# Optimization experiments

Measured on AMD Instinct MI355X. Metric: run time of the kernel, lower is better.

## Reference

```python
import jax, jax.numpy as jnp
import numpy as np

DEPTH = 6
H = 12
D = 768
FF = 4 * D
OUT_INDICES = (2, 5)
EPS = 1e-5


def layernorm(x, g, b):
    m = jnp.mean(x, axis=-1, keepdims=True)
    v = jnp.mean(jnp.square(x - m), axis=-1, keepdims=True)
    return (x - m) * jax.lax.rsqrt(v + EPS) * g + b


def setup_inputs() -> dict:
    key = jax.random.key(0)
    ks = jax.random.split(key, 8)
    B, N = 2, 1024
    s = 0.02
    inp = {
        "x": jax.random.normal(ks[0], (B, N, D), dtype=jnp.float32),
        "rel_bias": jax.random.normal(ks[1], (H, N, N), dtype=jnp.float32),
        "ln1_g": jnp.ones((DEPTH, D), jnp.float32),
        "ln1_b": jnp.zeros((DEPTH, D), jnp.float32),
        "qkv_w": jax.random.normal(ks[2], (DEPTH, D, 3 * D), dtype=jnp.float32) * s,
        "out_w": jax.random.normal(ks[3], (DEPTH, D, D), dtype=jnp.float32) * s,
        "out_b": jnp.zeros((DEPTH, D), jnp.float32),
        "ln2_g": jnp.ones((DEPTH, D), jnp.float32),
        "ln2_b": jnp.zeros((DEPTH, D), jnp.float32),
        "ff1_w": jax.random.normal(ks[4], (DEPTH, D, FF), dtype=jnp.float32) * s,
        "ff1_b": jnp.zeros((DEPTH, FF), jnp.float32),
        "ff2_w": jax.random.normal(ks[5], (DEPTH, FF, D), dtype=jnp.float32) * s,
        "ff2_b": jnp.zeros((DEPTH, D), jnp.float32),
        "lnf_g": jnp.ones((D,), jnp.float32),
        "lnf_b": jnp.zeros((D,), jnp.float32),
    }
    return inp


def reference(x, rel_bias, ln1_g, ln1_b, qkv_w, out_w, out_b, ln2_g, ln2_b,
              ff1_w, ff1_b, ff2_w, ff2_b, lnf_g, lnf_b):
    B, N, Dm = x.shape
    Dh = Dm // H
    scale = Dh ** -0.5
    kside = int(round(N ** 0.5))  # N is a perfect square (patch grid)
    feats = []
    for i in range(DEPTH):
        # --- attention block ---
        h = layernorm(x, ln1_g[i], ln1_b[i])
        qkv = h @ qkv_w[i]                                   # [B,N,3D]
        q, k, v = jnp.split(qkv, 3, axis=-1)
        q = q.reshape(B, N, H, Dh).transpose(0, 2, 1, 3)     # [B,H,N,Dh]
        k = k.reshape(B, N, H, Dh).transpose(0, 2, 1, 3)
        v = v.reshape(B, N, H, Dh).transpose(0, 2, 1, 3)
        scores = jnp.einsum('bhid,bhjd->bhij', q, k) * scale + rel_bias
        attn = jax.nn.softmax(scores, axis=-1)
        o = jnp.einsum('bhij,bhjd->bhid', attn, v)
        o = o.transpose(0, 2, 1, 3).reshape(B, N, Dm)
        x = x + (o @ out_w[i] + out_b[i])
        # --- FFN block ---
        h2 = layernorm(x, ln2_g[i], ln2_b[i])
        ff = jax.nn.gelu(h2 @ ff1_w[i] + ff1_b[i], approximate=False)
        x = x + (ff @ ff2_w[i] + ff2_b[i])
        if i in OUT_INDICES:
            feats.append(x.reshape(B, kside, kside, Dm).transpose(0, 3, 1, 2))
    xf = layernorm(x, lnf_g, lnf_b)
    return (xf, *feats)
```

## Files before the change

### kernel.cpp

```cpp
#include <hip/hip_runtime.h>
#include <hip/hip_bf16.h>

typedef unsigned short ushort_t;
typedef __attribute__((ext_vector_type(8))) __bf16 bf16x8;
typedef __attribute__((ext_vector_type(8))) unsigned short u16x8;
typedef __attribute__((ext_vector_type(4))) float f32x4;
typedef __attribute__((ext_vector_type(4))) unsigned int u32x4;

#define DEPTH 6
#define HEADS 12
#define DMODEL 768
#define FFDIM 3072
#define BATCH 2
#define SEQ 1024
#define ROWS (BATCH * SEQ)

static __device__ __forceinline__ ushort_t f2bf(float f) {
  unsigned u = __builtin_bit_cast(unsigned, f);
  u += 0x7fffu + ((u >> 16) & 1u);
  return (ushort_t)(u >> 16);
}
static __device__ __forceinline__ float bf2f(ushort_t v) {
  return __builtin_bit_cast(float, (unsigned)v << 16);
}

template <int MREP, int NREP, int EPI>
__global__ __launch_bounds__(256) void gemm_bt(
    const ushort_t* __restrict__ A, const ushort_t* __restrict__ Bt,
    int lda, int ldb, int K,
    void* __restrict__ out0, void* __restrict__ out1,
    const float* __restrict__ f0) {
  constexpr int BM = 32 * MREP;
  constexpr int BN = 32 * NREP;
  constexpr int CHA = BM / 32;
  constexpr int CHB = BN / 32;
  __shared__ ushort_t sA[2][BM * 64];
  __shared__ ushort_t sB[2][BN * 64];

  const int tid = threadIdx.x;
  const int lane = tid & 63;
  const int wid = tid >> 6;
  const int wm = wid >> 1, wn = wid & 1;

  int bx, by;
  {
    const int nb = gridDim.x * gridDim.y;
    const int bid = blockIdx.y * gridDim.x + blockIdx.x;
    const int q = nb >> 3;
    const int swz = (bid & 7) * q + (bid >> 3);
    bx = swz % gridDim.x;
    by = swz / gridDim.x;
  }

  const ushort_t* Ab = A + (long)bx * BM * lda;
  const ushort_t* Bb = Bt + (long)by * BN * ldb;

  const int srow = lane >> 3;
  const int scol = ((lane & 7) ^ srow) * 8;

  f32x4 acc[MREP][NREP];
#pragma unroll
  for (int m = 0; m < MREP; ++m)
#pragma unroll
    for (int n = 0; n < NREP; ++n) acc[m][n] = (f32x4){0.f, 0.f, 0.f, 0.f};

  const int fr = lane & 15;
  const int kq4 = lane >> 4;

  auto stage_tile = [&](int buf, int t) {
    const int k0 = t * 64;
#pragma unroll
    for (int j = 0; j < CHA; ++j) {
      const int c = wid * CHA + j;
      const ushort_t* src = Ab + (long)(c * 8 + srow) * lda + k0 + scol;
      __builtin_amdgcn_global_load_lds(
          (const __attribute__((address_space(1))) void*)src,
          (__attribute__((address_space(3))) void*)&sA[buf][c * 512], 16, 0, 0);
    }
#pragma unroll
    for (int j = 0; j < CHB; ++j) {
      const int c = wid * CHB + j;
      const ushort_t* src = Bb + (long)(c * 8 + srow) * ldb + k0 + scol;
      __builtin_amdgcn_global_load_lds(
          (const __attribute__((address_space(1))) void*)src,
          (__attribute__((address_space(3))) void*)&sB[buf][c * 512], 16, 0, 0);
    }
  };

  const int nt = K / 64;
  stage_tile(0, 0);
  for (int t = 0; t < nt; ++t) {
    const int cur = t & 1;
    asm volatile("s_waitcnt vmcnt(0)" ::: "memory");
    __builtin_amdgcn_s_barrier();
    if (t + 1 < nt) stage_tile(cur ^ 1, t + 1);
#pragma unroll
    for (int kk = 0; kk < 2; ++kk) {
      bf16x8 af[MREP], bfr[NREP];
#pragma unroll
      for (int m = 0; m < MREP; ++m) {
        const int row = wm * (MREP * 16) + m * 16 + fr;
        const int ch = (kk * 4 + kq4) ^ (row & 7);
        af[m] = *(const bf16x8*)&sA[cur][row * 64 + ch * 8];
      }
#pragma unroll
      for (int n = 0; n < NREP; ++n) {
        const int row = wn * (NREP * 16) + n * 16 + fr;
        const int ch = (kk * 4 + kq4) ^ (row & 7);
        bfr[n] = *(const bf16x8*)&sB[cur][row * 64 + ch * 8];
      }
#pragma unroll
      for (int m = 0; m < MREP; ++m)
#pragma unroll
        for (int n = 0; n < NREP; ++n)
          acc[m][n] = __builtin_amdgcn_mfma_f32_16x16x32_bf16(
              af[m], bfr[n], acc[m][n], 0, 0, 0);
    }
  }

  const long grow0 = (long)bx * BM + wm * (MREP * 16);
  const long gcol0 = (long)by * BN + wn * (NREP * 16);
  const int rr = (lane >> 4) * 4;
  const int cc = lane & 15;

#pragma unroll
  for (int m = 0; m < MREP; ++m) {
#pragma unroll
    for (int n = 0; n < NREP; ++n) {
#pragma unroll
      for (int r = 0; r < 4; ++r) {
        long row = grow0 + m * 16 + rr + r;
        long col = gcol0 + n * 16 + cc;
        float c = acc[m][n][r];
        if (EPI == 0) {
          ushort_t bv = f2bf(c);
          if (col < 1536) {
            ((ushort_t*)out0)[row * 2304 + col] = bv;
          } else {
            long h = (col - 1536) >> 6, d = (col - 1536) & 63;
            long b = row >> 10, i = row & 1023;
            ((ushort_t*)out1)[(((b * HEADS) + h) * 64 + d) * 1024 + i] = bv;
          }
        } else if (EPI == 3) {
          long idx = row * DMODEL + col;
          ((float*)out0)[idx] += c + f0[col];
        } else if (EPI == 4) {
          float t = c + f0[col];
          float g = 0.5f * t * (1.0f + erff(t * 0.70710678118f));
          ((ushort_t*)out0)[row * FFDIM + col] = f2bf(g);
        } else if (EPI == 5) {
          long idx = row * DMODEL + col;
          ((float*)out0)[idx] += c + f0[col];
        }
      }
    }
  }
}

__global__ __launch_bounds__(256) void pack_bias(const float* __restrict__ rel,
                                                 ushort_t* __restrict__ pb) {
  __shared__ ushort_t tile[1024];
  const int blk = blockIdx.x;
  const int t = blk & 15, qi = (blk >> 4) & 63, h = blk >> 10;
  const float* src = rel + ((size_t)h << 20) + (size_t)(qi * 16) * 1024 + t * 64;
  const int tid = threadIdx.x;
  const int kk = tid & 63;
#pragma unroll
  for (int it = 0; it < 4; ++it) {
    const int qr = (tid >> 6) * 4 + it;
    const float v = src[(size_t)qr * 1024 + kk];
    const int lane = (qr >> 2) * 16 + (kk & 15);
    const int idx = (kk >> 4) * 4 + (qr & 3);
    tile[lane * 16 + idx] = f2bf(v);
  }
  __syncthreads();
  ushort_t* dst = pb + (size_t)blk * 1024;
#pragma unroll
  for (int it = 0; it < 4; ++it) dst[it * 256 + tid] = tile[it * 256 + tid];
}

__global__ __launch_bounds__(128) void flash_attn(
    const ushort_t* __restrict__ qkv,
    const ushort_t* __restrict__ vt,
    const ushort_t* __restrict__ pbias,
    ushort_t* __restrict__ o) {
  __shared__ ushort_t sK[2][64 * 64];
  __shared__ ushort_t sV[2][64 * 64];
  __shared__ ushort_t sP[32 * 64];

  const int tid = threadIdx.x;
  const int lane = tid & 63;
  const int wid = tid >> 6;
  const int h = blockIdx.y, b = blockIdx.z;
  const int q0 = blockIdx.x * 32;
  const int qi = blockIdx.x * 2 + wid;

  const int fr = lane & 15;
  const int kq4 = lane >> 4;
  const int rr = kq4 * 4;
  const int cc = fr;

  const int srow = lane >> 3;
  const int scol = ((lane & 7) ^ srow) * 8;

  const ushort_t* qbase =
      qkv + (size_t)(b * 1024 + q0 + wid * 16 + fr) * 2304 + h * 64;
  bf16x8 qreg[2];
  qreg[0] = *(const bf16x8*)&qbase[kq4 * 8];
  qreg[1] = *(const bf16x8*)&qbase[32 + kq4 * 8];

  const ushort_t* Kbase = qkv + (size_t)(b * 1024) * 2304 + 768 + h * 64;
  const ushort_t* Vbase = vt + (size_t)((b * HEADS + h) * 64) * 1024;
  const ushort_t* pbb = pbias + (((size_t)h * 64 + qi) << 14) + lane * 16;

  f32x4 acc_o[4];
  float m_run[4], l_run[4];
#pragma unroll
  for (int n = 0; n < 4; ++n) acc_o[n] = (f32x4){0.f, 0.f, 0.f, 0.f};
#pragma unroll
  for (int r = 0; r < 4; ++r) { m_run[r] = -1e30f; l_run[r] = 0.f; }

  auto stage_kv = [&](int buf, int t) {
#pragma unroll
    for (int j = 0; j < 4; ++j) {
      const int c = wid * 4 + j;
      const ushort_t* src = Kbase + (size_t)(t * 64 + c * 8 + srow) * 2304 + scol;
      __builtin_amdgcn_global_load_lds(
          (const __attribute__((address_space(1))) void*)src,
          (__attribute__((address_space(3))) void*)&sK[buf][c * 512], 16, 0, 0);
    }
#pragma unroll
    for (int j = 0; j < 4; ++j) {
      const int c = wid * 4 + j;
      const ushort_t* src = Vbase + (size_t)(c * 8 + srow) * 1024 + t * 64 + scol;
      __builtin_amdgcn_global_load_lds(
          (const __attribute__((address_space(1))) void*)src,
          (__attribute__((address_space(3))) void*)&sV[buf][c * 512], 16, 0, 0);
    }
  };

  auto step = [&](int t, u16x8& bc0, u16x8& bc1, u16x8& bn0, u16x8& bn1) {
    const int cur = t & 1;
    asm volatile("s_waitcnt vmcnt(0)" ::: "memory");
    __builtin_amdgcn_s_barrier();
    if (t + 1 < 16) {
      stage_kv(cur ^ 1, t + 1);
      const ushort_t* pp = pbb + (size_t)(t + 1) * 1024;
      bn0 = *(const u16x8*)pp;
      bn1 = *(const u16x8*)(pp + 8);
    }

    f32x4 s[4];
#pragma unroll
    for (int n = 0; n < 4; ++n) s[n] = (f32x4){0.f, 0.f, 0.f, 0.f};
#pragma unroll
    for (int kk = 0; kk < 2; ++kk) {
#pragma unroll
      for (int n = 0; n < 4; ++n) {
        const int row = n * 16 + fr;
        const int ch = (kk * 4 + kq4) ^ (row & 7);
        bf16x8 kf = *(const bf16x8*)&sK[cur][row * 64 + ch * 8];
        s[n] =
            __builtin_amdgcn_mfma_f32_16x16x32_bf16(qreg[kk], kf, s[n], 0, 0, 0);
      }
    }

    float mr[4];
#pragma unroll
    for (int r = 0; r < 4; ++r) mr[r] = -1e30f;
#pragma unroll
    for (int n = 0; n < 4; ++n)
#pragma unroll
      for (int r = 0; r < 4; ++r) {
        const int idx = n * 4 + r;
        const float bv = bf2f(idx < 8 ? bc0[idx] : bc1[idx - 8]);
        float v = s[n][r] * 0.125f + bv;
        s[n][r] = v;
        mr[r] = fmaxf(mr[r], v);
      }
#pragma unroll
    for (int o_ = 1; o_ < 16; o_ <<= 1)
#pragma unroll
      for (int r = 0; r < 4; ++r) mr[r] = fmaxf(mr[r], __shfl_xor(mr[r], o_));

    float escale[4], psum[4];
#pragma unroll
    for (int r = 0; r < 4; ++r) {
      float mn = fmaxf(m_run[r], mr[r]);
      escale[r] = __expf(m_run[r] - mn);
      m_run[r] = mn;
      psum[r] = 0.f;
    }
#pragma unroll
    for (int n = 0; n < 4; ++n)
#pragma unroll
      for (int r = 0; r < 4; ++r) {
        float p = __expf(s[n][r] - m_run[r]);
        psum[r] += p;
        const int prow = wid * 16 + rr + r;
        const int pcol = n * 16 + cc;
        sP[prow * 64 + (((pcol >> 3) ^ (prow & 7)) << 3) + (pcol & 7)] = f2bf(p);
      }
#pragma unroll
    for (int o_ = 1; o_ < 16; o_ <<= 1)
#pragma unroll
      for (int r = 0; r < 4; ++r) psum[r] += __shfl_xor(psum[r], o_);
#pragma unroll
    for (int r = 0; r < 4; ++r) l_run[r] = l_run[r] * escale[r] + psum[r];

    asm volatile("s_waitcnt lgkmcnt(0)" ::: "memory");
    __builtin_amdgcn_s_barrier();

#pragma unroll
    for (int n = 0; n < 4; ++n)
#pragma unroll
      for (int r = 0; r < 4; ++r) acc_o[n][r] *= escale[r];
#pragma unroll
    for (int kk = 0; kk < 2; ++kk) {
      const int prow = wid * 16 + fr;
      const int pch = (kk * 4 + kq4) ^ (prow & 7);
      bf16x8 pf = *(const bf16x8*)&sP[prow * 64 + pch * 8];
#pragma unroll
      for (int n = 0; n < 4; ++n) {
        const int vrow = n * 16 + fr;
        const int vch = (kk * 4 + kq4) ^ (vrow & 7);
        bf16x8 vf = *(const bf16x8*)&sV[cur][vrow * 64 + vch * 8];
        acc_o[n] =
            __builtin_amdgcn_mfma_f32_16x16x32_bf16(pf, vf, acc_o[n], 0, 0, 0);
      }
    }
  };

  u16x8 bA0, bA1, bB0, bB1;
  bA0 = *(const u16x8*)pbb;
  bA1 = *(const u16x8*)(pbb + 8);
  stage_kv(0, 0);
  for (int tt = 0; tt < 16; tt += 2) {
    step(tt, bA0, bA1, bB0, bB1);
    step(tt + 1, bB0, bB1, bA0, bA1);
  }

  ushort_t* ob = o + (size_t)(b * 1024 + q0 + wid * 16) * 768 + h * 64;
#pragma unroll
  for (int r = 0; r < 4; ++r) {
    const float rinv = 1.f / l_run[r];
#pragma unroll
    for (int n = 0; n < 4; ++n)
      ob[(size_t)(rr + r) * 768 + n * 16 + cc] = f2bf(acc_o[n][r] * rinv);
  }
}

__global__ __launch_bounds__(256) void transpose_cast(
    const float* __restrict__ in, ushort_t* __restrict__ out, int R, int C) {
  __shared__ float t[32][33];
  const float* ip = in + (long)blockIdx.z * R * C;
  ushort_t* op = out + (long)blockIdx.z * R * C;
  int c0 = blockIdx.x * 32, r0 = blockIdx.y * 32;
  int tx = threadIdx.x;
  for (int i = threadIdx.y; i < 32; i += 8)
    t[i][tx] = ip[(long)(r0 + i) * C + c0 + tx];
  __syncthreads();
  for (int i = threadIdx.y; i < 32; i += 8)
    op[(long)(c0 + i) * R + r0 + tx] = f2bf(t[tx][i]);
}

__global__ __launch_bounds__(256) void ln_kernel(
    const float* __restrict__ x, const float* __restrict__ g,
    const float* __restrict__ b, void* __restrict__ out, int out_f32) {
  int row = blockIdx.x;
  int tid = threadIdx.x;
  int lane = tid & 63, wid = tid >> 6;
  const float* xr = x + (long)row * DMODEL;
  float v0 = xr[tid], v1 = xr[tid + 256], v2 = xr[tid + 512];
  float s = v0 + v1 + v2;
  __shared__ float red[8];
  for (int o = 32; o; o >>= 1) s += __shfl_xor(s, o);
  if (!lane) red[wid] = s;
  __syncthreads();
  float mean = (red[0] + red[1] + red[2] + red[3]) * (1.f / 768.f);
  float d0 = v0 - mean, d1 = v1 - mean, d2 = v2 - mean;
  float q = d0 * d0 + d1 * d1 + d2 * d2;
  for (int o = 32; o; o >>= 1) q += __shfl_xor(q, o);
  if (!lane) red[4 + wid] = q;
  __syncthreads();
  float var = (red[4] + red[5] + red[6] + red[7]) * (1.f / 768.f);
  float rs = rsqrtf(var + 1e-5f);
  float y0 = d0 * rs * g[tid] + b[tid];
  float y1 = d1 * rs * g[tid + 256] + b[tid + 256];
  float y2 = d2 * rs * g[tid + 512] + b[tid + 512];
  if (out_f32) {
    float* o_ = (float*)out + (long)row * DMODEL;
    o_[tid] = y0; o_[tid + 256] = y1; o_[tid + 512] = y2;
  } else {
    ushort_t* o_ = (ushort_t*)out + (long)row * DMODEL;
    o_[tid] = f2bf(y0); o_[tid + 256] = f2bf(y1); o_[tid + 512] = f2bf(y2);
  }
}

__global__ __launch_bounds__(256) void feat_kernel(const float* __restrict__ x,
                                                   float* __restrict__ out) {
  __shared__ float t[32][33];
  const float* xp = x + (long)blockIdx.z * SEQ * DMODEL;
  float* op = out + (long)blockIdx.z * DMODEL * SEQ;
  int n0 = blockIdx.x * 32, c0 = blockIdx.y * 32;
  int tx = threadIdx.x;
  for (int i = threadIdx.y; i < 32; i += 8)
    t[i][tx] = xp[(long)(n0 + i) * DMODEL + c0 + tx];
  __syncthreads();
  for (int i = threadIdx.y; i < 32; i += 8)
    op[(long)(c0 + i) * SEQ + n0 + tx] = t[tx][i];
}

extern "C" void kernel_launch(void* const* d_in, const int* in_sizes, int n_in,
                              void* d_out, int out_size, void* d_ws,
                              size_t ws_size, hipStream_t stream) {
  const float* x_in   = (const float*)d_in[0];
  const float* rel    = (const float*)d_in[1];
  const float* ln1_g  = (const float*)d_in[2];
  const float* ln1_b  = (const float*)d_in[3];
  const float* qkv_w  = (const float*)d_in[4];
  const float* out_w  = (const float*)d_in[5];
  const float* out_b  = (const float*)d_in[6];
  const float* ln2_g  = (const float*)d_in[7];
  const float* ln2_b  = (const float*)d_in[8];
  const float* ff1_w  = (const float*)d_in[9];
  const float* ff1_b  = (const float*)d_in[10];
  const float* ff2_w  = (const float*)d_in[11];
  const float* ff2_b  = (const float*)d_in[12];
  const float* lnf_g  = (const float*)d_in[13];
  const float* lnf_b  = (const float*)d_in[14];
  float* out = (float*)d_out;

  char* w = (char*)d_ws;
  ushort_t* wq_t = (ushort_t*)w; w += (size_t)DEPTH * 2304 * 768 * 2;
  ushort_t* wo_t = (ushort_t*)w; w += (size_t)DEPTH * 768 * 768 * 2;
  ushort_t* wf1_t = (ushort_t*)w; w += (size_t)DEPTH * 3072 * 768 * 2;
  ushort_t* wf2_t = (ushort_t*)w; w += (size_t)DEPTH * 768 * 3072 * 2;
  float* xb = (float*)w; w += (size_t)ROWS * DMODEL * 4;
  ushort_t* hb = (ushort_t*)w; w += (size_t)ROWS * DMODEL * 2;
  ushort_t* qkvb = (ushort_t*)w; w += (size_t)ROWS * 2304 * 2;
  ushort_t* vt = (ushort_t*)w; w += (size_t)BATCH * HEADS * 64 * 1024 * 2;
  ushort_t* ob = (ushort_t*)w; w += (size_t)ROWS * DMODEL * 2;
  ushort_t* ffb = (ushort_t*)w; w += (size_t)ROWS * FFDIM * 2;
  ushort_t* pbias = (ushort_t*)w; w += (size_t)HEADS * 1024 * 1024 * 2;

  dim3 tb(32, 8);
  transpose_cast<<<dim3(2304 / 32, 768 / 32, DEPTH), tb, 0, stream>>>(
      qkv_w, wq_t, 768, 2304);
  transpose_cast<<<dim3(768 / 32, 768 / 32, DEPTH), tb, 0, stream>>>(
      out_w, wo_t, 768, 768);
  transpose_cast<<<dim3(3072 / 32, 768 / 32, DEPTH), tb, 0, stream>>>(
      ff1_w, wf1_t, 768, 3072);
  transpose_cast<<<dim3(768 / 32, 3072 / 32, DEPTH), tb, 0, stream>>>(
      ff2_w, wf2_t, 3072, 768);
  pack_bias<<<HEADS * 64 * 16, 256, 0, stream>>>(rel, pbias);

  hipMemcpyAsync(xb, x_in, (size_t)ROWS * DMODEL * 4, hipMemcpyDeviceToDevice,
                 stream);

  for (int i = 0; i < DEPTH; ++i) {
    ln_kernel<<<ROWS, 256, 0, stream>>>(xb, ln1_g + i * 768, ln1_b + i * 768,
                                        hb, 0);
    gemm_bt<2, 2, 0><<<dim3(32, 36), 256, 0, stream>>>(
        hb, wq_t + (size_t)i * 2304 * 768, 768, 768, 768, qkvb, vt, nullptr);
    flash_attn<<<dim3(32, HEADS, BATCH), 128, 0, stream>>>(qkvb, vt, pbias, ob);
    gemm_bt<1, 2, 3><<<dim3(64, 12), 256, 0, stream>>>(
        ob, wo_t + (size_t)i * 768 * 768, 768, 768, 768, xb, nullptr,
        out_b + i * 768);
    ln_kernel<<<ROWS, 256, 0, stream>>>(xb, ln2_g + i * 768, ln2_b + i * 768,
                                        hb, 0);
    gemm_bt<2, 2, 4><<<dim3(32, 48), 256, 0, stream>>>(
        hb, wf1_t + (size_t)i * 3072 * 768, 768, 768, 768, ffb, nullptr,
        ff1_b + i * 3072);
    gemm_bt<1, 2, 5><<<dim3(64, 12), 256, 0, stream>>>(
        ffb, wf2_t + (size_t)i * 768 * 3072, 3072, 3072, 3072, xb, nullptr,
        ff2_b + i * 768);
    if (i == 2)
      feat_kernel<<<dim3(32, 24, 2), tb, 0, stream>>>(xb, out + 1572864);
    if (i == 5)
      feat_kernel<<<dim3(32, 24, 2), tb, 0, stream>>>(xb, out + 2 * 1572864);
  }
  ln_kernel<<<ROWS, 256, 0, stream>>>(xb, lnf_g, lnf_b, out, 1);
}
```

Before: 928.0 us.

## Split flash attention over KV halves and add a combine kernel

Flash attention now splits the key/value sequence into two halves across the grid's z dimension, doubling the number of blocks. Each half writes unnormalized fp32 partial outputs plus running max and sum to workspace. A new combine kernel merges the two halves with log-sum-exp rescaling and writes the bf16 output. This targets low occupancy in the attention kernel, at the cost of extra global traffic and an additional launch per layer.

```diff
diff --git a/kernel.cpp b/kernel.cpp
--- a/kernel.cpp
+++ b/kernel.cpp
@@ -183,7 +183,8 @@
     const ushort_t* __restrict__ qkv,
     const ushort_t* __restrict__ vt,
     const ushort_t* __restrict__ pbias,
-    ushort_t* __restrict__ o) {
+    float* __restrict__ o_part,
+    float* __restrict__ mlb) {
   __shared__ ushort_t sK[2][64 * 64];
   __shared__ ushort_t sV[2][64 * 64];
   __shared__ ushort_t sP[32 * 64];
@@ -191,7 +192,10 @@
   const int tid = threadIdx.x;
   const int lane = tid & 63;
   const int wid = tid >> 6;
-  const int h = blockIdx.y, b = blockIdx.z;
+  const int h = blockIdx.y;
+  const int b = blockIdx.z >> 1;
+  const int split = blockIdx.z & 1;
+  const int t0 = split * 8;
   const int q0 = blockIdx.x * 32;
   const int qi = blockIdx.x * 2 + wid;
 
@@ -243,7 +247,7 @@
     const int cur = t & 1;
     asm volatile("s_waitcnt vmcnt(0)" ::: "memory");
     __builtin_amdgcn_s_barrier();
-    if (t + 1 < 16) {
+    if (t + 1 < t0 + 8) {
       stage_kv(cur ^ 1, t + 1);
       const ushort_t* pp = pbb + (size_t)(t + 1) * 1024;
       bn0 = *(const u16x8*)pp;
@@ -332,21 +336,54 @@
   };
 
   u16x8 bA0, bA1, bB0, bB1;
-  bA0 = *(const u16x8*)pbb;
-  bA1 = *(const u16x8*)(pbb + 8);
-  stage_kv(0, 0);
-  for (int tt = 0; tt < 16; tt += 2) {
-    step(tt, bA0, bA1, bB0, bB1);
-    step(tt + 1, bB0, bB1, bA0, bA1);
-  }
-
-  ushort_t* ob = o + (size_t)(b * 1024 + q0 + wid * 16) * 768 + h * 64;
+  {
+    const ushort_t* pp = pbb + (size_t)t0 * 1024;
+    bA0 = *(const u16x8*)pp;
+    bA1 = *(const u16x8*)(pp + 8);
+  }
+  stage_kv(0, t0);
+  for (int tt = 0; tt < 8; tt += 2) {
+    step(t0 + tt, bA0, bA1, bB0, bB1);
+    step(t0 + tt + 1, bB0, bB1, bA0, bA1);
+  }
+
+  float* op = o_part + ((size_t)split * ROWS + b * 1024 + q0 + wid * 16) * 768 +
+              h * 64;
 #pragma unroll
   for (int r = 0; r < 4; ++r) {
-    const float rinv = 1.f / l_run[r];
 #pragma unroll
     for (int n = 0; n < 4; ++n)
-      ob[(size_t)(rr + r) * 768 + n * 16 + cc] = f2bf(acc_o[n][r] * rinv);
+      op[(size_t)(rr + r) * 768 + n * 16 + cc] = acc_o[n][r];
+  }
+  if (cc == 0) {
+#pragma unroll
+    for (int r = 0; r < 4; ++r) {
+      const size_t row = (size_t)b * 1024 + q0 + wid * 16 + rr + r;
+      float* mp = mlb + (((size_t)split * ROWS + row) * HEADS + h) * 2;
+      mp[0] = m_run[r];
+      mp[1] = l_run[r];
+    }
+  }
+}
+
+__global__ __launch_bounds__(256) void flash_combine(
+    const float* __restrict__ o_part, const float* __restrict__ mlb,
+    ushort_t* __restrict__ o) {
+  const size_t row = blockIdx.x;
+  const int tid = threadIdx.x;
+#pragma unroll
+  for (int i = 0; i < 3; ++i) {
+    const int col = tid + i * 256;
+    const int h = col >> 6;
+    const float* mp0 = mlb + (row * HEADS + h) * 2;
+    const float* mp1 = mlb + (((size_t)ROWS + row) * HEADS + h) * 2;
+    const float m0 = mp0[0], l0 = mp0[1];
+    const float m1 = mp1[0], l1 = mp1[1];
+    const float m = fmaxf(m0, m1);
+    const float e0 = __expf(m0 - m), e1 = __expf(m1 - m);
+    const float a0 = o_part[row * 768 + col];
+    const float a1 = o_part[((size_t)ROWS + row) * 768 + col];
+    o[row * 768 + col] = f2bf((e0 * a0 + e1 * a1) / (e0 * l0 + e1 * l1));
   }
 }
 
@@ -443,6 +480,8 @@
   ushort_t* ob = (ushort_t*)w; w += (size_t)ROWS * DMODEL * 2;
   ushort_t* ffb = (ushort_t*)w; w += (size_t)ROWS * FFDIM * 2;
   ushort_t* pbias = (ushort_t*)w; w += (size_t)HEADS * 1024 * 1024 * 2;
+  float* opart = (float*)w; w += (size_t)2 * ROWS * DMODEL * 4;
+  float* mlb = (float*)w; w += (size_t)2 * ROWS * HEADS * 2 * 4;
 
   dim3 tb(32, 8);
   transpose_cast<<<dim3(2304 / 32, 768 / 32, DEPTH), tb, 0, stream>>>(
@@ -463,7 +502,9 @@
                                         hb, 0);
     gemm_bt<2, 2, 0><<<dim3(32, 36), 256, 0, stream>>>(
         hb, wq_t + (size_t)i * 2304 * 768, 768, 768, 768, qkvb, vt, nullptr);
-    flash_attn<<<dim3(32, HEADS, BATCH), 128, 0, stream>>>(qkvb, vt, pbias, ob);
+    flash_attn<<<dim3(32, HEADS, BATCH * 2), 128, 0, stream>>>(qkvb, vt, pbias,
+                                                               opart, mlb);
+    flash_combine<<<ROWS, 256, 0, stream>>>(opart, mlb, ob);
     gemm_bt<1, 2, 3><<<dim3(64, 12), 256, 0, stream>>>(
         ob, wo_t + (size_t)i * 768 * 768, 768, 768, 768, xb, nullptr,
         out_b + i * 768);
```

After: 997.4 us. 7.5% more time.

## Triple-buffer K/V and bias prefetch in flash attention with two-tile lookahead

Applied to the files above, without the earlier changes.

Changes the flash attention K/V LDS staging from double to triple buffering and prefetches the bias registers two tiles ahead. A partial vmcnt(10) wait replaces the full vmcnt(0) drain, so loads for the next tile stay in flight while the current tile computes. The main loop is fully unrolled so buffer indices are compile-time constants. This raises LDS use per block, which may lower occupancy, and correctness depends on the vmcnt count matching the number of outstanding loads.

```diff
diff --git a/kernel.cpp b/kernel.cpp
--- a/kernel.cpp
+++ b/kernel.cpp
@@ -184,8 +184,8 @@
     const ushort_t* __restrict__ vt,
     const ushort_t* __restrict__ pbias,
     ushort_t* __restrict__ o) {
-  __shared__ ushort_t sK[2][64 * 64];
-  __shared__ ushort_t sV[2][64 * 64];
+  __shared__ ushort_t sK[3][64 * 64];
+  __shared__ ushort_t sV[3][64 * 64];
   __shared__ ushort_t sP[32 * 64];
 
   const int tid = threadIdx.x;
@@ -220,6 +220,13 @@
 #pragma unroll
   for (int r = 0; r < 4; ++r) { m_run[r] = -1e30f; l_run[r] = 0.f; }
 
+  u16x8 bR0[3], bR1[3];
+
+  auto load_bias = [&](int slot, int t) {
+    const ushort_t* pp = pbb + (size_t)t * 1024;
+    bR0[slot] = *(const u16x8*)pp;
+    bR1[slot] = *(const u16x8*)(pp + 8);
+  };
   auto stage_kv = [&](int buf, int t) {
 #pragma unroll
     for (int j = 0; j < 4; ++j) {
@@ -239,15 +246,22 @@
     }
   };
 
-  auto step = [&](int t, u16x8& bc0, u16x8& bc1, u16x8& bn0, u16x8& bn1) {
-    const int cur = t & 1;
-    asm volatile("s_waitcnt vmcnt(0)" ::: "memory");
+  load_bias(0, 0);
+  stage_kv(0, 0);
+  load_bias(1, 1);
+  stage_kv(1, 1);
+
+#pragma unroll
+  for (int t = 0; t < 16; ++t) {
+    const int cur = t % 3;
+    if (t < 15)
+      asm volatile("s_waitcnt vmcnt(10)" ::: "memory");
+    else
+      asm volatile("s_waitcnt vmcnt(0)" ::: "memory");
     __builtin_amdgcn_s_barrier();
-    if (t + 1 < 16) {
-      stage_kv(cur ^ 1, t + 1);
-      const ushort_t* pp = pbb + (size_t)(t + 1) * 1024;
-      bn0 = *(const u16x8*)pp;
-      bn1 = *(const u16x8*)(pp + 8);
+    if (t + 2 < 16) {
+      load_bias((t + 2) % 3, t + 2);
+      stage_kv((t + 2) % 3, t + 2);
     }
 
     f32x4 s[4];
@@ -273,7 +287,7 @@
 #pragma unroll
       for (int r = 0; r < 4; ++r) {
         const int idx = n * 4 + r;
-        const float bv = bf2f(idx < 8 ? bc0[idx] : bc1[idx - 8]);
+        const float bv = bf2f(idx < 8 ? bR0[cur][idx] : bR1[cur][idx - 8]);
         float v = s[n][r] * 0.125f + bv;
         s[n][r] = v;
         mr[r] = fmaxf(mr[r], v);
@@ -329,15 +343,6 @@
             __builtin_amdgcn_mfma_f32_16x16x32_bf16(pf, vf, acc_o[n], 0, 0, 0);
       }
     }
-  };
-
-  u16x8 bA0, bA1, bB0, bB1;
-  bA0 = *(const u16x8*)pbb;
-  bA1 = *(const u16x8*)(pbb + 8);
-  stage_kv(0, 0);
-  for (int tt = 0; tt < 16; tt += 2) {
-    step(tt, bA0, bA1, bB0, bB1);
-    step(tt + 1, bB0, bB1, bA0, bA1);
   }
 
   ushort_t* ob = o + (size_t)(b * 1024 + q0 + wid * 16) * 768 + h * 64;
```

Measured after the change: 1.091 ms. 1.18x slower.
